# Kernel tuning notes

Measured on AMD Instinct MI355X. Metric: run time of the kernel, lower is better.

Reference implementation:

```python
import jax, jax.numpy as jnp
import numpy as np

BLOCK_H, BLOCK_W = 8, 8
IMG_H, IMG_W = 256, 512
NBLOCKS = 256
NSEQ = 256
BATCH = 16
TILES = (IMG_H // BLOCK_H) * (IMG_W // BLOCK_W)  # 2048
TAU = 1.0


def gen_deblocking_lut():
    l = np.zeros((3, 3, 3), np.float32)
    l[2, 0, 0] = 1.0
    l[1, 0, 1] = 1.0; l[2, 0, 1] = 2.0
    l[0, 0, 2] = 1.0; l[1, 0, 2] = 1.0; l[2, 0, 2] = 2.0
    l[1, 1, 0] = 1.0; l[2, 1, 0] = 2.0
    l[0, 1, 1] = 1.0; l[1, 1, 1] = 1.0; l[2, 1, 1] = 2.0
    l[0, 1, 2] = 1.0; l[1, 1, 2] = 2.0; l[2, 1, 2] = 2.0
    l[0, 2, 0] = 1.0; l[1, 2, 0] = 1.0; l[2, 2, 0] = 2.0
    l[0, 2, 1] = 1.0; l[1, 2, 1] = 2.0; l[2, 2, 1] = 2.0
    l[0, 2, 2] = 1.0; l[1, 2, 2] = 2.0; l[2, 2, 2] = 2.0
    return jnp.asarray(l)


def trilinear_interp(lut, x, y, z):
    # lut: (3,3,3); x,y,z: same shape, floats (indices clamped like torch version)
    x0 = jnp.clip(jnp.floor(x), 0, 1).astype(jnp.int32)
    y0 = jnp.clip(jnp.floor(y), 0, 1).astype(jnp.int32)
    z0 = jnp.clip(jnp.floor(z), 0, 1).astype(jnp.int32)
    x1 = jnp.clip(x0 + 1, 0, 2)
    y1 = jnp.clip(y0 + 1, 0, 2)
    z1 = jnp.clip(z0 + 1, 0, 2)
    xd = x - x0.astype(x.dtype)
    yd = y - y0.astype(y.dtype)
    zd = z - z0.astype(z.dtype)
    c000 = lut[x0, y0, z0]; c100 = lut[x1, y0, z0]
    c010 = lut[x0, y1, z0]; c110 = lut[x1, y1, z0]
    c001 = lut[x0, y0, z1]; c101 = lut[x1, y0, z1]
    c011 = lut[x0, y1, z1]; c111 = lut[x1, y1, z1]
    c00 = c000 * (1 - xd) * (1 - yd) + c100 * xd * (1 - yd) + c010 * (1 - xd) * yd + c110 * xd * yd
    c01 = c001 * (1 - xd) * (1 - yd) + c101 * xd * (1 - yd) + c011 * (1 - xd) * yd + c111 * xd * yd
    return c00 * (1 - zd) + c01 * zd


def deblocking_filter(img_raw, lut):
    # Faithful port, including the source quirks: second pass reuses `center`
    # (pre-filter image) in the LUT lookup and shifts along W, not H.
    img = img_raw * 2
    B, C, H, W = img.shape
    xm = jnp.arange(W) % BLOCK_W
    ym = jnp.arange(H) % BLOCK_H
    mask_x = ((xm == 0) | (xm == BLOCK_W - 1)).reshape(1, 1, 1, W)
    mask_y = ((ym == 0) | (ym == BLOCK_H - 1)).reshape(1, 1, H, 1)
    padded = jnp.pad(img, ((0, 0), (0, 0), (1, 1), (1, 1)), mode='edge')
    center = padded[:, :, 1:-1, 1:-1]
    left = padded[:, :, 1:-1, :-2]
    right = padded[:, :, 1:-1, 2:]
    filtered = jnp.where(mask_x, trilinear_interp(lut, center, left, right), center)
    padded2 = jnp.pad(filtered, ((0, 0), (0, 0), (1, 1), (1, 1)), mode='edge')
    center2 = padded2[:, :, 1:-1, 1:-1]
    up = padded2[:, :, 1:-1, :-2]
    down = padded2[:, :, 1:-1, 2:]
    filtered2 = jnp.where(mask_y, trilinear_interp(lut, center, up, down), center2)
    return filtered2 / 2


def setup_inputs() -> dict:
    key = jax.random.key(0)
    k1, k2, k3, k4 = jax.random.split(key, 4)
    sequence = jax.random.normal(k1, (NSEQ, TILES, NBLOCKS), dtype=jnp.float32)
    blocks = jax.random.normal(k2, (NBLOCKS, BLOCK_H, BLOCK_W), dtype=jnp.float32)
    gumbel = jax.random.gumbel(k3, (BATCH, TILES, NBLOCKS), dtype=jnp.float32)
    frame_idxs = jax.random.randint(k4, (BATCH,), 0, NSEQ)
    lut = gen_deblocking_lut()
    return {"sequence": sequence, "blocks": blocks, "lut": lut,
            "gumbel": gumbel, "frame_idxs": frame_idxs}


def reference(sequence, blocks, lut, gumbel, frame_idxs):
    # Training branch: soft gumbel-softmax over the codebook per tile.
    logits = sequence[frame_idxs]                       # [B, T, N]
    block_weights = jax.nn.softmax((logits + gumbel) / TAU, axis=-1)
    block_len = BLOCK_H * BLOCK_W
    # soft codebook lookup, already permuted: [B, block_len, T]
    uf = jnp.einsum('btn,nk->bkt', block_weights, blocks.reshape(NBLOCKS, block_len))
    Hb, Wb = IMG_H // BLOCK_H, IMG_W // BLOCK_W
    # Fold (non-overlapping, stride == kernel)
    rec = uf.reshape(-1, BLOCK_H, BLOCK_W, Hb, Wb)
    rec = rec.transpose(0, 3, 1, 4, 2).reshape(-1, 1, IMG_H, IMG_W)
    return deblocking_filter(rec, lut)
```

## Files before the change

### kernel.cpp

```cpp
#include <hip/hip_runtime.h>


#define NB       256
#define TIL      2048
#define EPITCH   264
#define ROWPITCH 520

typedef short  s8v __attribute__((ext_vector_type(8)));
typedef float  f4v __attribute__((ext_vector_type(4)));

__device__ __forceinline__ unsigned short f2bf(float f) {
    unsigned int u = __float_as_uint(f);
    u += 0x7fffu + ((u >> 16) & 1u);
    return (unsigned short)(u >> 16);
}

__device__ __forceinline__ unsigned int pk2(float a, float b) {
    return (unsigned int)f2bf(a) | ((unsigned int)f2bf(b) << 16);
}

__device__ __forceinline__ float4 ldnt4(const float* p) {
    float4 v;
    v.x = __builtin_nontemporal_load(p + 0);
    v.y = __builtin_nontemporal_load(p + 1);
    v.z = __builtin_nontemporal_load(p + 2);
    v.w = __builtin_nontemporal_load(p + 3);
    return v;
}

__device__ __forceinline__ float trilerp(const float* __restrict__ lutS,
                                         float x, float y, float z) {
    int x0 = (int)fminf(fmaxf(floorf(x), 0.0f), 1.0f);
    int y0 = (int)fminf(fmaxf(floorf(y), 0.0f), 1.0f);
    int z0 = (int)fminf(fmaxf(floorf(z), 0.0f), 1.0f);
    float xd = x - (float)x0;
    float yd = y - (float)y0;
    float zd = z - (float)z0;
    int base = x0 * 9 + y0 * 3 + z0;
    float c000 = lutS[base],     c100 = lutS[base + 9];
    float c010 = lutS[base + 3], c110 = lutS[base + 12];
    float c001 = lutS[base + 1], c101 = lutS[base + 10];
    float c011 = lutS[base + 4], c111 = lutS[base + 13];
    float xm = 1.0f - xd, ym = 1.0f - yd;
    float c00 = c000 * xm * ym + c100 * xd * ym + c010 * xm * yd + c110 * xd * yd;
    float c01 = c001 * xm * ym + c101 * xd * ym + c011 * xm * yd + c111 * xd * yd;
    return c00 * (1.0f - zd) + c01 * zd;
}

__device__ __forceinline__ float fval(const float* __restrict__ row,
                                      const float* __restrict__ fcolr, int x) {
    int x8 = x & 7;
    if (x8 == 0 || x8 == 7) return fcolr[(x >> 3) * 2 + (x8 == 7)];
    return row[x];
}

__global__ __launch_bounds__(512, 4)
void ImageReconstruction_46523085751029_kernel(
        const float* __restrict__ seq,
        const float* __restrict__ blocks,
        const float* __restrict__ lut,
        const float* __restrict__ gumbel,
        const int*   __restrict__ fidx,
        float*       __restrict__ out)
{
    __shared__ __align__(16) unsigned short E[64 * EPITCH];
    __shared__ float lutS[28];

    const int t    = threadIdx.x;
    const int lane = t & 63;
    const int wave = t >> 6;
    const int ws   = wave & 3;
    const int mh   = wave >> 2;
    const int b    = blockIdx.x >> 5;
    const int hb   = blockIdx.x & 31;

    if (t < 27) lutS[t] = lut[t];

    const int f = fidx[b];
    const float* sp = seq    + (size_t)f * (TIL * NB) + (size_t)hb * (64 * NB);
    const float* gp = gumbel + (size_t)b * (TIL * NB) + (size_t)hb * (64 * NB);

    float4 lq[8], gq[8];
    #pragma unroll
    for (int r = 0; r < 8; ++r)
        lq[r] = ldnt4(sp + (r * 512 + t) * 4);
    #pragma unroll
    for (int r = 0; r < 8; ++r)
        gq[r] = ldnt4(gp + (r * 512 + t) * 4);

    #pragma unroll
    for (int r = 0; r < 8; ++r) {
        int fi = r * 512 + t;
        int tile = fi >> 6;
        int n    = (fi & 63) * 4;
        unsigned int u0 = pk2(__expf(lq[r].x + gq[r].x), __expf(lq[r].y + gq[r].y));
        unsigned int u1 = pk2(__expf(lq[r].z + gq[r].z), __expf(lq[r].w + gq[r].w));
        *(uint2*)&E[tile * EPITCH + n] = make_uint2(u0, u1);
    }

    const int g = lane >> 4;
    const int c = lane & 15;
    const float* bp = blocks + ws * 16 + c;
    s8v bfrag[8];
    #pragma unroll
    for (int ks = 0; ks < 8; ++ks) {
        int k0 = ks * 32 + g * 8;
        unsigned int u[4];
        #pragma unroll
        for (int jj = 0; jj < 4; ++jj)
            u[jj] = pk2(bp[(k0 + 2 * jj) * 64], bp[(k0 + 2 * jj + 1) * 64]);
        int4 iv = make_int4(u[0], u[1], u[2], u[3]);
        bfrag[ks] = __builtin_bit_cast(s8v, iv);
    }
    s8v ones;
    {
        unsigned int uo = (c == 0) ? 0x3F803F80u : 0u;
        int4 iv = make_int4(uo, uo, uo, uo);
        ones = __builtin_bit_cast(s8v, iv);
    }

    __syncthreads();

    f4v acc[2], accd[2];
    #pragma unroll
    for (int mi = 0; mi < 2; ++mi) { acc[mi] = (f4v)0.0f; accd[mi] = (f4v)0.0f; }

    #pragma unroll
    for (int ks = 0; ks < 8; ++ks) {
        #pragma unroll
        for (int mi = 0; mi < 2; ++mi) {
            int mt = mh * 2 + mi;
            s8v a = *(const s8v*)&E[(mt * 16 + c) * EPITCH + ks * 32 + g * 8];
            acc[mi]  = __builtin_amdgcn_mfma_f32_16x16x32_bf16(a, bfrag[ks], acc[mi],  0, 0, 0);
            accd[mi] = __builtin_amdgcn_mfma_f32_16x16x32_bf16(a, ones,      accd[mi], 0, 0, 0);
        }
    }

    __syncthreads();

    float* rows_img = (float*)E;
    float* fcol     = (float*)E + 8 * ROWPITCH;

    #pragma unroll
    for (int mi = 0; mi < 2; ++mi) {
        #pragma unroll
        for (int rg = 0; rg < 4; ++rg) {
            float den = __shfl(accd[mi][rg], (lane >> 4) * 16);
            float val = acc[mi][rg] * (2.0f / den);
            int row = (mh * 2 + mi) * 16 + g * 4 + rg;
            int p   = ws * 16 + c;
            int bh  = p >> 3, bw = p & 7;
            rows_img[bh * ROWPITCH + row * 8 + bw] = val;
        }
    }
    __syncthreads();

    #pragma unroll
    for (int it = 0; it < 2; ++it) {
        int idx = it * 512 + t;
        int bh = idx >> 7, ci = idx & 127;
        int w  = (ci >> 1) * 8 + ((ci & 1) ? 7 : 0);
        const float* row = rows_img + bh * ROWPITCH;
        int wm = (w > 0)   ? w - 1 : 0;
        int wp = (w < 511) ? w + 1 : 511;
        fcol[bh * 128 + ci] = trilerp(lutS, row[w], row[wm], row[wp]);
    }
    __syncthreads();

    float* op = out + (size_t)b * (256 * 512) + (size_t)hb * (8 * 512);
    #pragma unroll 2
    for (int it = 0; it < 8; ++it) {
        int pix = it * 512 + t;
        int bh = pix >> 9, w = pix & 511;
        const float* row = rows_img + bh * ROWPITCH;
        const float* fr  = fcol + bh * 128;
        float gv;
        if (bh == 0 || bh == 7) {
            int wm = (w > 0)   ? w - 1 : 0;
            int wp = (w < 511) ? w + 1 : 511;
            gv = trilerp(lutS, row[w], fval(row, fr, wm), fval(row, fr, wp));
        } else {
            gv = fval(row, fr, w);
        }
        __builtin_nontemporal_store(0.5f * gv, op + bh * 512 + w);
    }
}

extern "C" void kernel_launch(void* const* d_in, const int* in_sizes, int n_in,
                              void* d_out, int out_size, void* d_ws, size_t ws_size,
                              hipStream_t stream) {
    const float* seq    = (const float*)d_in[0];
    const float* blocks = (const float*)d_in[1];
    const float* lut    = (const float*)d_in[2];
    const float* gumbel = (const float*)d_in[3];
    const int*   fidx   = (const int*)d_in[4];
    float* out = (float*)d_out;

    dim3 grid(512);
    dim3 block(512);
    ImageReconstruction_46523085751029_kernel<<<grid, block, 0, stream>>>(
        seq, blocks, lut, gumbel, fidx, out);
}
```

Measured before the change: 21.21 us.

## Split each image row-band across two half-width blocks with halo tiles

Each workgroup now handles half of an 8-row band (32 tiles, 256 columns) with 256 threads, and the grid doubles to 1024 blocks. This is meant to raise occupancy and parallelism on the device. Wave 0 recomputes one neighbouring tile's boundary columns in fp32 as a halo, so the horizontal deblocking stays correct across the split. The cost is redundant halo loads, extra reductions and more complex boundary logic.

New measurement: 25.77 us. +21.4%, slower.

```diff
diff --git a/kernel.cpp b/kernel.cpp
--- a/kernel.cpp
+++ b/kernel.cpp
@@ -1,10 +1,11 @@
 #include <hip/hip_runtime.h>
 
 
-#define NB       256
-#define TIL      2048
-#define EPITCH   264
-#define ROWPITCH 520
+#define NB     256
+#define TIL    2048
+#define EPITCH 264
+#define RP     264
+#define FP     66
 
 typedef short  s8v __attribute__((ext_vector_type(8)));
 typedef float  f4v __attribute__((ext_vector_type(4)));
@@ -47,14 +48,7 @@
     return c00 * (1.0f - zd) + c01 * zd;
 }
 
-__device__ __forceinline__ float fval(const float* __restrict__ row,
-                                      const float* __restrict__ fcolr, int x) {
-    int x8 = x & 7;
-    if (x8 == 0 || x8 == 7) return fcolr[(x >> 3) * 2 + (x8 == 7)];
-    return row[x];
-}
-
-__global__ __launch_bounds__(512, 4)
+__global__ __launch_bounds__(256, 4)
 void ImageReconstruction_46523085751029_kernel(
         const float* __restrict__ seq,
         const float* __restrict__ blocks,
@@ -63,34 +57,37 @@
         const int*   __restrict__ fidx,
         float*       __restrict__ out)
 {
-    __shared__ __align__(16) unsigned short E[64 * EPITCH];
+    __shared__ __align__(16) unsigned short E[32 * EPITCH];
+    __shared__ float halo[8][2];
+    __shared__ float fcolX[8];
     __shared__ float lutS[28];
 
     const int t    = threadIdx.x;
     const int lane = t & 63;
     const int wave = t >> 6;
-    const int ws   = wave & 3;
-    const int mh   = wave >> 2;
-    const int b    = blockIdx.x >> 5;
-    const int hb   = blockIdx.x & 31;
+    const int bid  = blockIdx.x;
+    const int b    = bid >> 6;
+    const int hb   = (bid >> 1) & 31;
+    const int half = bid & 1;
 
     if (t < 27) lutS[t] = lut[t];
 
     const int f = fidx[b];
-    const float* sp = seq    + (size_t)f * (TIL * NB) + (size_t)hb * (64 * NB);
-    const float* gp = gumbel + (size_t)b * (TIL * NB) + (size_t)hb * (64 * NB);
+    const size_t rowbase = (size_t)(hb * 64 + half * 32) * NB;
+    const float* sp = seq    + (size_t)f * (TIL * NB) + rowbase;
+    const float* gp = gumbel + (size_t)b * (TIL * NB) + rowbase;
 
     float4 lq[8], gq[8];
     #pragma unroll
     for (int r = 0; r < 8; ++r)
-        lq[r] = ldnt4(sp + (r * 512 + t) * 4);
+        lq[r] = ldnt4(sp + (r * 256 + t) * 4);
     #pragma unroll
     for (int r = 0; r < 8; ++r)
-        gq[r] = ldnt4(gp + (r * 512 + t) * 4);
+        gq[r] = ldnt4(gp + (r * 256 + t) * 4);
 
     #pragma unroll
     for (int r = 0; r < 8; ++r) {
-        int fi = r * 512 + t;
+        int fi = r * 256 + t;
         int tile = fi >> 6;
         int n    = (fi & 63) * 4;
         unsigned int u0 = pk2(__expf(lq[r].x + gq[r].x), __expf(lq[r].y + gq[r].y));
@@ -98,9 +95,44 @@
         *(uint2*)&E[tile * EPITCH + n] = make_uint2(u0, u1);
     }
 
+    if (wave == 0) {
+        const int hwb = half ? 31 : 32;
+        const size_t hbase = (size_t)(hb * 64 + hwb) * NB + lane * 4;
+        float4 s4 = *(const float4*)(seq    + (size_t)f * (TIL * NB) + hbase);
+        float4 g4 = *(const float4*)(gumbel + (size_t)b * (TIL * NB) + hbase);
+        float e0 = __expf(s4.x + g4.x), e1 = __expf(s4.y + g4.y);
+        float e2 = __expf(s4.z + g4.z), e3 = __expf(s4.w + g4.w);
+        float den = e0 + e1 + e2 + e3;
+        #pragma unroll
+        for (int m = 1; m < 64; m <<= 1) den += __shfl_xor(den, m);
+        const int c0 = half ? 6 : 0;
+        const int n0 = lane * 4;
+        float pk[16];
+        #pragma unroll
+        for (int bh2 = 0; bh2 < 8; ++bh2) {
+            const float* bb = blocks + bh2 * 8 + c0;
+            float2 q0 = *(const float2*)(bb + (n0 + 0) * 64);
+            float2 q1 = *(const float2*)(bb + (n0 + 1) * 64);
+            float2 q2 = *(const float2*)(bb + (n0 + 2) * 64);
+            float2 q3 = *(const float2*)(bb + (n0 + 3) * 64);
+            pk[bh2 * 2 + 0] = e0 * q0.x + e1 * q1.x + e2 * q2.x + e3 * q3.x;
+            pk[bh2 * 2 + 1] = e0 * q0.y + e1 * q1.y + e2 * q2.y + e3 * q3.y;
+        }
+        #pragma unroll
+        for (int i = 0; i < 16; ++i) {
+            #pragma unroll
+            for (int m = 1; m < 64; m <<= 1) pk[i] += __shfl_xor(pk[i], m);
+        }
+        if (lane == 0) {
+            float sc = 2.0f / den;
+            #pragma unroll
+            for (int i = 0; i < 16; ++i) halo[i >> 1][i & 1] = pk[i] * sc;
+        }
+    }
+
     const int g = lane >> 4;
     const int c = lane & 15;
-    const float* bp = blocks + ws * 16 + c;
+    const float* bp = blocks + wave * 16 + c;
     s8v bfrag[8];
     #pragma unroll
     for (int ks = 0; ks < 8; ++ks) {
@@ -129,8 +161,7 @@
     for (int ks = 0; ks < 8; ++ks) {
         #pragma unroll
         for (int mi = 0; mi < 2; ++mi) {
-            int mt = mh * 2 + mi;
-            s8v a = *(const s8v*)&E[(mt * 16 + c) * EPITCH + ks * 32 + g * 8];
+            s8v a = *(const s8v*)&E[(mi * 16 + c) * EPITCH + ks * 32 + g * 8];
             acc[mi]  = __builtin_amdgcn_mfma_f32_16x16x32_bf16(a, bfrag[ks], acc[mi],  0, 0, 0);
             accd[mi] = __builtin_amdgcn_mfma_f32_16x16x32_bf16(a, ones,      accd[mi], 0, 0, 0);
         }
@@ -139,7 +170,7 @@
     __syncthreads();
 
     float* rows_img = (float*)E;
-    float* fcol     = (float*)E + 8 * ROWPITCH;
+    float* fcol     = (float*)E + 8 * RP;
 
     #pragma unroll
     for (int mi = 0; mi < 2; ++mi) {
@@ -147,42 +178,68 @@
         for (int rg = 0; rg < 4; ++rg) {
             float den = __shfl(accd[mi][rg], (lane >> 4) * 16);
             float val = acc[mi][rg] * (2.0f / den);
-            int row = (mh * 2 + mi) * 16 + g * 4 + rg;
-            int p   = ws * 16 + c;
-            int bh  = p >> 3, bw = p & 7;
-            rows_img[bh * ROWPITCH + row * 8 + bw] = val;
+            int tl = mi * 16 + g * 4 + rg;
+            int p  = wave * 16 + c;
+            int bh2 = p >> 3, bw = p & 7;
+            rows_img[bh2 * RP + tl * 8 + bw] = val;
         }
     }
     __syncthreads();
 
     #pragma unroll
     for (int it = 0; it < 2; ++it) {
-        int idx = it * 512 + t;
-        int bh = idx >> 7, ci = idx & 127;
-        int w  = (ci >> 1) * 8 + ((ci & 1) ? 7 : 0);
-        const float* row = rows_img + bh * ROWPITCH;
-        int wm = (w > 0)   ? w - 1 : 0;
-        int wp = (w < 511) ? w + 1 : 511;
-        fcol[bh * 128 + ci] = trilerp(lutS, row[w], row[wm], row[wp]);
-    }
-    __syncthreads();
-
-    float* op = out + (size_t)b * (256 * 512) + (size_t)hb * (8 * 512);
+        int idx = it * 256 + t;
+        int bh2 = idx >> 6, ci = idx & 63;
+        int tl = ci >> 1, side = ci & 1;
+        int wl = tl * 8 + side * 7;
+        int wg = half * 256 + wl;
+        int wmg = (wg > 0)   ? wg - 1 : 0;
+        int wpg = (wg < 511) ? wg + 1 : 511;
+        int lm = wmg - half * 256, lp = wpg - half * 256;
+        const float* row = rows_img + bh2 * RP;
+        float cx = row[wl];
+        float cy = (lm < 0) ? halo[bh2][2 + lm] : (lm > 255 ? halo[bh2][lm - 256] : row[lm]);
+        float cz = (lp < 0) ? halo[bh2][2 + lp] : (lp > 255 ? halo[bh2][lp - 256] : row[lp]);
+        fcol[bh2 * FP + ci] = trilerp(lutS, cx, cy, cz);
+    }
+    if (t < 8) {
+        if (half == 0)
+            fcolX[t] = trilerp(lutS, halo[t][0], rows_img[t * RP + 255], halo[t][1]);
+        else
+            fcolX[t] = trilerp(lutS, halo[t][1], halo[t][0], rows_img[t * RP + 0]);
+    }
+    __syncthreads();
+
+    float* op = out + (size_t)b * (256 * 512) + (size_t)hb * (8 * 512) + half * 256;
     #pragma unroll 2
     for (int it = 0; it < 8; ++it) {
-        int pix = it * 512 + t;
-        int bh = pix >> 9, w = pix & 511;
-        const float* row = rows_img + bh * ROWPITCH;
-        const float* fr  = fcol + bh * 128;
+        int bh2 = it, wl = t;
+        int wg = half * 256 + wl;
+        const float* row = rows_img + bh2 * RP;
+        const float* fr  = fcol + bh2 * FP;
         float gv;
-        if (bh == 0 || bh == 7) {
-            int wm = (w > 0)   ? w - 1 : 0;
-            int wp = (w < 511) ? w + 1 : 511;
-            gv = trilerp(lutS, row[w], fval(row, fr, wm), fval(row, fr, wp));
+        if (bh2 == 0 || bh2 == 7) {
+            int wmg = (wg > 0)   ? wg - 1 : 0;
+            int wpg = (wg < 511) ? wg + 1 : 511;
+            float x = row[wl];
+            int m8 = wmg & 7;
+            float y = (m8 == 0 || m8 == 7)
+                    ? ((wmg - half * 256 < 0 || wmg - half * 256 > 255)
+                         ? fcolX[bh2]
+                         : fr[((wmg - half * 256) >> 3) * 2 + (m8 == 7)])
+                    : row[wmg - half * 256];
+            int p8 = wpg & 7;
+            float z = (p8 == 0 || p8 == 7)
+                    ? ((wpg - half * 256 < 0 || wpg - half * 256 > 255)
+                         ? fcolX[bh2]
+                         : fr[((wpg - half * 256) >> 3) * 2 + (p8 == 7)])
+                    : row[wpg - half * 256];
+            gv = trilerp(lutS, x, y, z);
         } else {
-            gv = fval(row, fr, w);
-        }
-        __builtin_nontemporal_store(0.5f * gv, op + bh * 512 + w);
+            int w8 = wl & 7;
+            gv = (w8 == 0 || w8 == 7) ? fr[(wl >> 3) * 2 + (w8 == 7)] : row[wl];
+        }
+        __builtin_nontemporal_store(0.5f * gv, op + bh2 * 512 + wl);
     }
 }
 
@@ -196,8 +253,8 @@
     const int*   fidx   = (const int*)d_in[4];
     float* out = (float*)d_out;
 
-    dim3 grid(512);
-    dim3 block(512);
+    dim3 grid(1024);
+    dim3 block(256);
     ImageReconstruction_46523085751029_kernel<<<grid, block, 0, stream>>>(
         seq, blocks, lut, gumbel, fidx, out);
 }
```

## Process two block-rows per workgroup with both rows' loads issued upfront

Applied to the files above, without the earlier changes.

Each workgroup now handles two consecutive 8-pixel block-rows instead of one, so the grid is halved to 256. Both rows' logits and gumbel data are loaded into registers at the start, and the codebook fragments are built once and shared by both rows. A separate LDS buffer is used for each row. The intent is to amortize the codebook setup and keep more memory traffic in flight per workgroup. In exchange it doubles register and LDS use, drops occupancy (launch bounds 2), and with only 256 workgroups may leave some of the CUs idle.

Result: slower. 22.19 us (+4.6%).

```diff
diff --git a/kernel.cpp b/kernel.cpp
--- a/kernel.cpp
+++ b/kernel.cpp
@@ -5,6 +5,7 @@
 #define TIL      2048
 #define EPITCH   264
 #define ROWPITCH 520
+#define EELEMS   (64 * EPITCH)
 
 typedef short  s8v __attribute__((ext_vector_type(8)));
 typedef float  f4v __attribute__((ext_vector_type(4)));
@@ -54,39 +55,15 @@
     return row[x];
 }
 
-__global__ __launch_bounds__(512, 4)
-void ImageReconstruction_46523085751029_kernel(
-        const float* __restrict__ seq,
-        const float* __restrict__ blocks,
-        const float* __restrict__ lut,
-        const float* __restrict__ gumbel,
-        const int*   __restrict__ fidx,
-        float*       __restrict__ out)
+__device__ __forceinline__ void process_row(
+        unsigned short* __restrict__ Erow,
+        const float4 (&lq)[8], const float4 (&gq)[8],
+        const s8v (&bfrag)[8], const s8v& ones,
+        float* __restrict__ op, const float* __restrict__ lutS,
+        int t, int lane, int wave, int ws, int mh)
 {
-    __shared__ __align__(16) unsigned short E[64 * EPITCH];
-    __shared__ float lutS[28];
-
-    const int t    = threadIdx.x;
-    const int lane = t & 63;
-    const int wave = t >> 6;
-    const int ws   = wave & 3;
-    const int mh   = wave >> 2;
-    const int b    = blockIdx.x >> 5;
-    const int hb   = blockIdx.x & 31;
-
-    if (t < 27) lutS[t] = lut[t];
-
-    const int f = fidx[b];
-    const float* sp = seq    + (size_t)f * (TIL * NB) + (size_t)hb * (64 * NB);
-    const float* gp = gumbel + (size_t)b * (TIL * NB) + (size_t)hb * (64 * NB);
-
-    float4 lq[8], gq[8];
-    #pragma unroll
-    for (int r = 0; r < 8; ++r)
-        lq[r] = ldnt4(sp + (r * 512 + t) * 4);
-    #pragma unroll
-    for (int r = 0; r < 8; ++r)
-        gq[r] = ldnt4(gp + (r * 512 + t) * 4);
+    const int g = lane >> 4;
+    const int c = lane & 15;
 
     #pragma unroll
     for (int r = 0; r < 8; ++r) {
@@ -95,51 +72,27 @@
         int n    = (fi & 63) * 4;
         unsigned int u0 = pk2(__expf(lq[r].x + gq[r].x), __expf(lq[r].y + gq[r].y));
         unsigned int u1 = pk2(__expf(lq[r].z + gq[r].z), __expf(lq[r].w + gq[r].w));
-        *(uint2*)&E[tile * EPITCH + n] = make_uint2(u0, u1);
-    }
-
-    const int g = lane >> 4;
-    const int c = lane & 15;
-    const float* bp = blocks + ws * 16 + c;
-    s8v bfrag[8];
-    #pragma unroll
-    for (int ks = 0; ks < 8; ++ks) {
-        int k0 = ks * 32 + g * 8;
-        unsigned int u[4];
-        #pragma unroll
-        for (int jj = 0; jj < 4; ++jj)
-            u[jj] = pk2(bp[(k0 + 2 * jj) * 64], bp[(k0 + 2 * jj + 1) * 64]);
-        int4 iv = make_int4(u[0], u[1], u[2], u[3]);
-        bfrag[ks] = __builtin_bit_cast(s8v, iv);
-    }
-    s8v ones;
-    {
-        unsigned int uo = (c == 0) ? 0x3F803F80u : 0u;
-        int4 iv = make_int4(uo, uo, uo, uo);
-        ones = __builtin_bit_cast(s8v, iv);
-    }
-
+        *(uint2*)&Erow[tile * EPITCH + n] = make_uint2(u0, u1);
+    }
     __syncthreads();
 
     f4v acc[2], accd[2];
     #pragma unroll
     for (int mi = 0; mi < 2; ++mi) { acc[mi] = (f4v)0.0f; accd[mi] = (f4v)0.0f; }
-
     #pragma unroll
     for (int ks = 0; ks < 8; ++ks) {
         #pragma unroll
         for (int mi = 0; mi < 2; ++mi) {
             int mt = mh * 2 + mi;
-            s8v a = *(const s8v*)&E[(mt * 16 + c) * EPITCH + ks * 32 + g * 8];
+            s8v a = *(const s8v*)&Erow[(mt * 16 + c) * EPITCH + ks * 32 + g * 8];
             acc[mi]  = __builtin_amdgcn_mfma_f32_16x16x32_bf16(a, bfrag[ks], acc[mi],  0, 0, 0);
             accd[mi] = __builtin_amdgcn_mfma_f32_16x16x32_bf16(a, ones,      accd[mi], 0, 0, 0);
         }
     }
-
-    __syncthreads();
-
-    float* rows_img = (float*)E;
-    float* fcol     = (float*)E + 8 * ROWPITCH;
+    __syncthreads();
+
+    float* rows_img = (float*)Erow;
+    float* fcol     = (float*)Erow + 8 * ROWPITCH;
 
     #pragma unroll
     for (int mi = 0; mi < 2; ++mi) {
@@ -167,7 +120,6 @@
     }
     __syncthreads();
 
-    float* op = out + (size_t)b * (256 * 512) + (size_t)hb * (8 * 512);
     #pragma unroll 2
     for (int it = 0; it < 8; ++it) {
         int pix = it * 512 + t;
@@ -186,6 +138,71 @@
     }
 }
 
+__global__ __launch_bounds__(512, 2)
+void ImageReconstruction_46523085751029_kernel(
+        const float* __restrict__ seq,
+        const float* __restrict__ blocks,
+        const float* __restrict__ lut,
+        const float* __restrict__ gumbel,
+        const int*   __restrict__ fidx,
+        float*       __restrict__ out)
+{
+    __shared__ __align__(16) unsigned short E[2][EELEMS];
+    __shared__ float lutS[28];
+
+    const int t    = threadIdx.x;
+    const int lane = t & 63;
+    const int wave = t >> 6;
+    const int ws   = wave & 3;
+    const int mh   = wave >> 2;
+    const int row0 = blockIdx.x * 2;
+    const int b    = row0 >> 5;
+    const int hb0  = row0 & 31;
+
+    if (t < 27) lutS[t] = lut[t];
+
+    const int f = fidx[b];
+    const float* sp = seq    + (size_t)f * (TIL * NB) + (size_t)(hb0 * 64) * NB;
+    const float* gp = gumbel + (size_t)b * (TIL * NB) + (size_t)(hb0 * 64) * NB;
+
+    float4 lqA[8], gqA[8], lqB[8], gqB[8];
+    #pragma unroll
+    for (int r = 0; r < 8; ++r) lqA[r] = ldnt4(sp + (r * 512 + t) * 4);
+    #pragma unroll
+    for (int r = 0; r < 8; ++r) gqA[r] = ldnt4(gp + (r * 512 + t) * 4);
+    #pragma unroll
+    for (int r = 0; r < 8; ++r) lqB[r] = ldnt4(sp + 16384 + (r * 512 + t) * 4);
+    #pragma unroll
+    for (int r = 0; r < 8; ++r) gqB[r] = ldnt4(gp + 16384 + (r * 512 + t) * 4);
+
+    const int g = lane >> 4;
+    const int c = lane & 15;
+    const float* bp = blocks + ws * 16 + c;
+    s8v bfrag[8];
+    #pragma unroll
+    for (int ks = 0; ks < 8; ++ks) {
+        int k0 = ks * 32 + g * 8;
+        unsigned int u[4];
+        #pragma unroll
+        for (int jj = 0; jj < 4; ++jj)
+            u[jj] = pk2(bp[(k0 + 2 * jj) * 64], bp[(k0 + 2 * jj + 1) * 64]);
+        int4 iv = make_int4(u[0], u[1], u[2], u[3]);
+        bfrag[ks] = __builtin_bit_cast(s8v, iv);
+    }
+    s8v ones;
+    {
+        unsigned int uo = (c == 0) ? 0x3F803F80u : 0u;
+        int4 iv = make_int4(uo, uo, uo, uo);
+        ones = __builtin_bit_cast(s8v, iv);
+    }
+
+    float* opA = out + (size_t)b * (256 * 512) + (size_t)hb0 * (8 * 512);
+    process_row(&E[0][0], lqA, gqA, bfrag, ones, opA, lutS, t, lane, wave, ws, mh);
+
+    float* opB = opA + 8 * 512;
+    process_row(&E[1][0], lqB, gqB, bfrag, ones, opB, lutS, t, lane, wave, ws, mh);
+}
+
 extern "C" void kernel_launch(void* const* d_in, const int* in_sizes, int n_in,
                               void* d_out, int out_size, void* d_ws, size_t ws_size,
                               hipStream_t stream) {
@@ -196,7 +213,7 @@
     const int*   fidx   = (const int*)d_in[4];
     float* out = (float*)d_out;
 
-    dim3 grid(512);
+    dim3 grid(256);
     dim3 block(512);
     ImageReconstruction_46523085751029_kernel<<<grid, block, 0, stream>>>(
         seq, blocks, lut, gumbel, fidx, out);
```
